# Kernel tuning notes

Hardware: AMD Instinct MI355X
Metric: run time of the kernel (lower is better)

## Reference

```python
import jax, jax.numpy as jnp
import numpy as np

B, T = 64, 1024
FRAME, ENC, HID = 512, 256, 512
LN_EPS = 1e-5


def setup_inputs() -> dict:
    key = jax.random.key(0)
    ks = jax.random.split(key, 16)
    s = 0.05
    return {
        "x": jax.random.normal(ks[0], (B, FRAME, T), jnp.float32),
        "states_hc": jax.random.normal(ks[1], (4, B, HID), jnp.float32) * s,
        "W_enc": jax.random.normal(ks[2], (ENC, FRAME), jnp.float32) * s,
        "ln_g": jnp.ones((ENC,), jnp.float32),
        "ln_b": jnp.zeros((ENC,), jnp.float32),
        "Wih1": jax.random.normal(ks[3], (4 * HID, ENC), jnp.float32) * s,
        "Whh1": jax.random.normal(ks[4], (4 * HID, HID), jnp.float32) * s,
        "bih1": jax.random.normal(ks[5], (4 * HID,), jnp.float32) * s,
        "bhh1": jax.random.normal(ks[6], (4 * HID,), jnp.float32) * s,
        "Wih2": jax.random.normal(ks[7], (4 * HID, HID), jnp.float32) * s,
        "Whh2": jax.random.normal(ks[8], (4 * HID, HID), jnp.float32) * s,
        "bih2": jax.random.normal(ks[9], (4 * HID,), jnp.float32) * s,
        "bhh2": jax.random.normal(ks[10], (4 * HID,), jnp.float32) * s,
        "Wlin": jax.random.normal(ks[11], (ENC, HID), jnp.float32) * s,
        "blin": jax.random.normal(ks[12], (ENC,), jnp.float32) * s,
        "W_dec": jax.random.normal(ks[13], (FRAME, ENC), jnp.float32) * s,
    }


def _lstm(x, h0, c0, Wih, Whh, bih, bhh):
    # x: [B,T,I]; PyTorch gate order i,f,g,o. Precompute input projections.
    pre = jnp.einsum("bti,gi->btg", x, Wih) + bih + bhh  # [B,T,4H]

    def step(carry, p):
        h, c = carry
        gates = p + h @ Whh.T
        i, f, g, o = jnp.split(gates, 4, axis=-1)
        c = jax.nn.sigmoid(f) * c + jax.nn.sigmoid(i) * jnp.tanh(g)
        h = jax.nn.sigmoid(o) * jnp.tanh(c)
        return (h, c), h

    (h, c), ys = jax.lax.scan(step, (h0, c0), pre.transpose(1, 0, 2))
    return ys.transpose(1, 0, 2), h, c  # [B,T,H]


def reference(x, states_hc, W_enc, ln_g, ln_b, Wih1, Whh1, bih1, bhh1,
              Wih2, Whh2, bih2, bhh2, Wlin, blin, W_dec):
    # encoder: conv1x1 over channels -> [B,ENC,T], then to [B,T,ENC]
    encoded = jnp.einsum("bct,oc->bto", x, W_enc)  # [B,T,ENC]
    mu = jnp.mean(encoded, axis=-1, keepdims=True)
    var = jnp.var(encoded, axis=-1, keepdims=True)
    enc_norm = (encoded - mu) / jnp.sqrt(var + LN_EPS) * ln_g + ln_b

    h1, c1 = states_hc[0], states_hc[1]
    h2, c2 = states_hc[2], states_hc[3]
    x1, h1, c1 = _lstm(enc_norm, h1, c1, Wih1, Whh1, bih1, bhh1)
    x2, h2, c2 = _lstm(x1, h2, c2, Wih2, Whh2, bih2, bhh2)
    # dropout is identity at inference
    mask = jax.nn.sigmoid(x2 @ Wlin.T + blin)  # [B,T,ENC]
    est = mask * encoded  # mask applied to un-normalized encoding
    decoded = jnp.einsum("bto,fo->bft", est, W_dec)  # [B,FRAME,T]
    states_out = jnp.stack([h1, c1, h2, c2], axis=0)  # [4,B,HID]
    return decoded, states_out
```

## Files before the change

kernel.cpp:

```cpp
#include <hip/hip_runtime.h>
#include <stdint.h>

#define B_ 64
#define T_ 1024
#define E_ 256
#define H_ 512
#define BH_ (B_*H_)
#define DEC_ELEMS ((size_t)B_*512*1024)

typedef __attribute__((ext_vector_type(8))) short bf16x8;
typedef __attribute__((ext_vector_type(4))) float f32x4;
typedef unsigned long long u64;

__device__ __forceinline__ unsigned short f2bf(float f) {
  union { float f; unsigned int u; } v; v.f = f;
  unsigned int r = (v.u + 0x7fffu + ((v.u >> 16) & 1u)) >> 16;
  return (unsigned short)r;
}
__device__ __forceinline__ float bf2f(unsigned short s) {
  union { float f; unsigned int u; } v; v.u = ((unsigned int)s) << 16;
  return v.f;
}
__device__ __forceinline__ float sigf(float x) { return 1.f/(1.f + __expf(-x)); }
__device__ __forceinline__ float tanhfast(float x) {
  float e = __expf(2.f*x);
  return 1.f - 2.f/(e + 1.f);
}
__device__ __forceinline__ void st4bf(unsigned short* p, float4 v) {
  ushort4 u; u.x=f2bf(v.x); u.y=f2bf(v.y); u.z=f2bf(v.z); u.w=f2bf(v.w);
  *(ushort4*)p = u;
}
__device__ __forceinline__ u64 ld_dc64(const unsigned short* p) {
  return __hip_atomic_load((const u64*)p, __ATOMIC_RELAXED, __HIP_MEMORY_SCOPE_AGENT);
}
__device__ __forceinline__ void st_dc64(unsigned short* p, u64 v) {
  __hip_atomic_store((u64*)p, v, __ATOMIC_RELAXED, __HIP_MEMORY_SCOPE_AGENT);
}

__device__ __forceinline__ void waitflags(const int* f, int target, int wv) {
  if ((threadIdx.x >> 6) == wv) {
    const int* p = f + (threadIdx.x & 63);
    for (;;) {
      int v = __hip_atomic_load(p, __ATOMIC_RELAXED, __HIP_MEMORY_SCOPE_AGENT);
      if (__all(v >= target)) break;
      __builtin_amdgcn_s_sleep(1);
    }
  }
  __syncthreads();
}

__global__ void k_prep(const float* __restrict__ Wenc, const float* __restrict__ Wlin,
                       const float* __restrict__ Wdec, const float* __restrict__ states,
                       unsigned short* __restrict__ wencb, unsigned short* __restrict__ wlinb,
                       unsigned short* __restrict__ wdecb,
                       unsigned short* h1bc, unsigned short* h2bc) {
  int i = blockIdx.x*256 + threadIdx.x;
  if (i < 131072) {
    wencb[i] = f2bf(Wenc[i]);
    wlinb[i] = f2bf(Wlin[i]);
    wdecb[i] = f2bf(Wdec[i]);
  }
  if (i < BH_/4) {
    float4 a  = *(const float4*)(states + (size_t)i*4);
    float4 b2 = *(const float4*)(states + (size_t)2*BH_ + (size_t)i*4);
    ushort4 ua; ua.x=f2bf(a.x);  ua.y=f2bf(a.y);  ua.z=f2bf(a.z);  ua.w=f2bf(a.w);
    ushort4 ub; ub.x=f2bf(b2.x); ub.y=f2bf(b2.y); ub.z=f2bf(b2.z); ub.w=f2bf(b2.w);
    st_dc64(&h1bc[BH_ + i*4], *(const u64*)&ua);
    st_dc64(&h2bc[BH_ + i*4], *(const u64*)&ub);
  }
}

__global__ __launch_bounds__(256) void k_enc(const float* __restrict__ x,
    const unsigned short* __restrict__ wencb, const float* __restrict__ lng,
    const float* __restrict__ lnb,
    unsigned short* __restrict__ enc_norm, unsigned short* __restrict__ encoded) {
  __shared__ __align__(16) unsigned short xs[16][520];
  __shared__ __align__(16) float es[16][265];
  const int bx = blockIdx.x;
  const int b = bx >> 6, tt = (bx & 63) << 4;
  const int tid = threadIdx.x;

  const float* xb = x + (size_t)b*512*1024 + tt;
  #pragma unroll
  for (int it = 0; it < 8; ++it) {
    int idx = tid + it*256;
    int c = idx >> 2, i4 = idx & 3;
    float4 v = *(const float4*)(xb + (size_t)c*1024 + i4*4);
    xs[i4*4+0][c]=f2bf(v.x); xs[i4*4+1][c]=f2bf(v.y);
    xs[i4*4+2][c]=f2bf(v.z); xs[i4*4+3][c]=f2bf(v.w);
  }
  __syncthreads();

  const int w = tid >> 6, lane = tid & 63;
  const int n16 = lane & 15, q = lane >> 4;
  f32x4 acc[4];
  #pragma unroll
  for (int i = 0; i < 4; ++i) acc[i] = (f32x4){0.f,0.f,0.f,0.f};
  for (int ks = 0; ks < 16; ++ks) {
    int k0 = ks*32 + q*8;
    bf16x8 af = *(const bf16x8*)&xs[n16][k0];
    #pragma unroll
    for (int i = 0; i < 4; ++i) {
      int o = (w*4+i)*16 + n16;
      bf16x8 bf = *(const bf16x8*)&wencb[(size_t)o*512 + k0];
      acc[i] = __builtin_amdgcn_mfma_f32_16x16x32_bf16(af, bf, acc[i], 0,0,0);
    }
  }
  #pragma unroll
  for (int i = 0; i < 4; ++i) {
    int o = (w*4+i)*16 + n16;
    #pragma unroll
    for (int r = 0; r < 4; ++r) es[q*4+r][o] = acc[i][r];
  }
  __syncthreads();

  const int tl = tid >> 4, l16 = tid & 15;
  float s = 0.f, ss = 0.f;
  #pragma unroll
  for (int k = 0; k < 16; ++k) { float v = es[tl][l16 + 16*k]; s += v; ss += v*v; }
  #pragma unroll
  for (int d = 1; d < 16; d <<= 1) { s += __shfl_xor(s, d, 64); ss += __shfl_xor(ss, d, 64); }
  float mu  = s  * (1.f/256.f);
  float var = ss * (1.f/256.f) - mu*mu;
  float rstd = rsqrtf(var + 1e-5f);
  #pragma unroll
  for (int k = 0; k < 16; ++k) {
    int o = l16 + 16*k;
    xs[tl][o] = f2bf((es[tl][o] - mu)*rstd*lng[o] + lnb[o]);
  }
  __syncthreads();
  #pragma unroll
  for (int it = 0; it < 2; ++it) {
    int idx = tid + it*256; int row = idx >> 5, ch = idx & 31;
    *(uint4*)&enc_norm[((size_t)(b*1024 + tt + row))*256 + ch*8] = *(const uint4*)&xs[row][ch*8];
  }
  __syncthreads();
  #pragma unroll
  for (int k = 0; k < 16; ++k) { int o = l16 + 16*k; xs[tl][o] = f2bf(es[tl][o]); }
  __syncthreads();
  #pragma unroll
  for (int it = 0; it < 2; ++it) {
    int idx = tid + it*256; int row = idx >> 5, ch = idx & 31;
    *(uint4*)&encoded[((size_t)(b*1024 + tt + row))*256 + ch*8] = *(const uint4*)&xs[row][ch*8];
  }
}

__global__ __launch_bounds__(256, 1) void k_recur(
    const float* __restrict__ states,
    const float* __restrict__ Wih1, const float* __restrict__ Whh1,
    const float* __restrict__ bih1, const float* __restrict__ bhh1,
    const float* __restrict__ Wih2, const float* __restrict__ Whh2,
    const float* __restrict__ bih2, const float* __restrict__ bhh2,
    const unsigned short* __restrict__ enc_norm,
    unsigned short* __restrict__ x2,
    unsigned short* h1bc, unsigned short* h2bc,
    int* flags1, int* flags2,
    float* __restrict__ out_states)
{
  __shared__ __align__(16) unsigned short wl1[32][776];
  __shared__ __align__(16) unsigned short wl2[32][1032];
  __shared__ __align__(16) unsigned short inA[16][1288];
  __shared__ float ps[2][32][17];
  __shared__ float cb[2][8][16];
  __shared__ float bias1[32], bias2[32];
  __shared__ __align__(8) unsigned short h1sh[16][8], h2sh[16][8];

  const int tid = threadIdx.x;
  const int g  = blockIdx.x & 3;
  const int j  = blockIdx.x >> 2;
  const int b0 = g*16;
  const int hc0 = j*8;
  int* f1 = flags1 + g*64;
  int* f2 = flags2 + g*64;

  for (int idx = tid; idx < 32*192; idx += 256) {
    int n = idx / 192, p = idx % 192;
    int R = (n>>3)*512 + hc0 + (n&7);
    if (p < 64) {
      st4bf(&wl1[n][p*4], *(const float4*)(Wih1 + (size_t)R*256 + p*4));
    } else {
      int p2 = p - 64;
      st4bf(&wl1[n][256 + p2*4], *(const float4*)(Whh1 + (size_t)R*512 + p2*4));
    }
  }
  for (int idx = tid; idx < 32*256; idx += 256) {
    int n = idx >> 8, p = idx & 255;
    int R = (n>>3)*512 + hc0 + (n&7);
    if (p < 128) {
      st4bf(&wl2[n][p*4], *(const float4*)(Wih2 + (size_t)R*512 + p*4));
    } else {
      int p2 = p - 128;
      st4bf(&wl2[n][512 + p2*4], *(const float4*)(Whh2 + (size_t)R*512 + p2*4));
    }
  }
  if (tid < 32) {
    int R = (tid>>3)*512 + hc0 + (tid&7);
    bias1[tid] = bih1[R] + bhh1[R];
    bias2[tid] = bih2[R] + bhh2[R];
  }
  if (tid < 128) {
    int b = tid & 15, hc = tid >> 4;
    cb[0][hc][b] = states[(size_t)1*BH_ + (b0+b)*H_ + hc0+hc];
    cb[1][hc][b] = states[(size_t)3*BH_ + (b0+b)*H_ + hc0+hc];
  }
  __syncthreads();

  const int w = tid >> 6, lane = tid & 63;
  const int n16 = lane & 15, q = lane >> 4;
  const int nt = w & 1, kh = w >> 1;

  for (int t = 0; t < T_; ++t) {
    const int pc = t & 1, pr = pc ^ 1;

    #pragma unroll
    for (int it = 0; it < 2; ++it) {
      int idx = tid + it*256;
      int b = idx >> 5, p = idx & 31;
      *(uint4*)&inA[b][p*8] = *(const uint4*)&enc_norm[((size_t)(b0+b)*T_ + t)*E_ + p*8];
    }
    if (t >= 1) waitflags(f1, t, 1);
    {
      u64 tmp[8];
      #pragma unroll
      for (int it = 0; it < 8; ++it) {
        int idx = tid + it*256; int b = idx >> 7, p = idx & 127;
        tmp[it] = ld_dc64(&h1bc[(size_t)pr*BH_ + (b0+b)*H_ + p*4]);
      }
      #pragma unroll
      for (int it = 0; it < 8; ++it) {
        int idx = tid + it*256; int b = idx >> 7, p = idx & 127;
        *(u64*)&inA[b][256 + p*4] = tmp[it];
      }
    }
    __syncthreads();

    {
      f32x4 acc = (f32x4){0.f,0.f,0.f,0.f};
      #pragma unroll
      for (int ks = 0; ks < 12; ++ks) {
        int k0 = kh*384 + ks*32 + q*8;
        bf16x8 af = *(const bf16x8*)&inA[n16][k0];
        bf16x8 bf = *(const bf16x8*)&wl1[nt*16 + n16][k0];
        acc = __builtin_amdgcn_mfma_f32_16x16x32_bf16(af, bf, acc, 0,0,0);
      }
      #pragma unroll
      for (int r = 0; r < 4; ++r) ps[kh][nt*16+n16][q*4+r] = acc[r];
    }
    __syncthreads();
    if (tid < 128) {
      int b = tid & 15, hc = tid >> 4;
      float ip = ps[0][hc][b]    + ps[1][hc][b]    + bias1[hc];
      float fp = ps[0][8+hc][b]  + ps[1][8+hc][b]  + bias1[8+hc];
      float gp = ps[0][16+hc][b] + ps[1][16+hc][b] + bias1[16+hc];
      float op = ps[0][24+hc][b] + ps[1][24+hc][b] + bias1[24+hc];
      float c = sigf(fp)*cb[0][hc][b] + sigf(ip)*tanhfast(gp);
      cb[0][hc][b] = c;
      float h = sigf(op)*tanhfast(c);
      h1sh[b][hc] = f2bf(h);
      if (t == T_-1) {
        out_states[(size_t)0*BH_ + (b0+b)*H_ + hc0+hc] = h;
        out_states[(size_t)1*BH_ + (b0+b)*H_ + hc0+hc] = c;
      }
    }
    __syncthreads();
    if (tid < 32) {
      int b = tid & 15, qq = tid >> 4;
      st_dc64(&h1bc[(size_t)pc*BH_ + (b0+b)*H_ + hc0 + qq*4], *(const u64*)&h1sh[b][qq*4]);
    }
    if (tid < 64) {
      asm volatile("s_waitcnt vmcnt(0)" ::: "memory");
      if (tid == 0)
        __hip_atomic_store(&f1[j], t+1, __ATOMIC_RELAXED, __HIP_MEMORY_SCOPE_AGENT);
    }

    if (t >= 2) waitflags(f2, t-1, 2);
    if (t >= 1) {
      u64 tmp[8];
      #pragma unroll
      for (int it = 0; it < 8; ++it) {
        int idx = tid + it*256; int b = idx >> 7, p = idx & 127;
        tmp[it] = ld_dc64(&h2bc[(size_t)pc*BH_ + (b0+b)*H_ + p*4]);
      }
      #pragma unroll
      for (int it = 0; it < 8; ++it) {
        int idx = tid + it*256; int b = idx >> 7, p = idx & 127;
        *(u64*)&inA[b][768 + p*4] = tmp[it];
      }
    }
    __syncthreads();

    if (t >= 1) {
      {
        f32x4 acc = (f32x4){0.f,0.f,0.f,0.f};
        #pragma unroll
        for (int ks = 0; ks < 16; ++ks) {
          int k0 = kh*512 + ks*32 + q*8;
          bf16x8 af = *(const bf16x8*)&inA[n16][256 + k0];
          bf16x8 bf = *(const bf16x8*)&wl2[nt*16 + n16][k0];
          acc = __builtin_amdgcn_mfma_f32_16x16x32_bf16(af, bf, acc, 0,0,0);
        }
        #pragma unroll
        for (int r = 0; r < 4; ++r) ps[kh][nt*16+n16][q*4+r] = acc[r];
      }
      __syncthreads();
      if (tid < 128) {
        int b = tid & 15, hc = tid >> 4;
        float ip = ps[0][hc][b]    + ps[1][hc][b]    + bias2[hc];
        float fp = ps[0][8+hc][b]  + ps[1][8+hc][b]  + bias2[8+hc];
        float gp = ps[0][16+hc][b] + ps[1][16+hc][b] + bias2[16+hc];
        float op = ps[0][24+hc][b] + ps[1][24+hc][b] + bias2[24+hc];
        float c = sigf(fp)*cb[1][hc][b] + sigf(ip)*tanhfast(gp);
        cb[1][hc][b] = c;
        float h = sigf(op)*tanhfast(c);
        h2sh[b][hc] = f2bf(h);
      }
      __syncthreads();
      if (tid < 32) {
        int b = tid & 15, qq = tid >> 4;
        u64 v = *(const u64*)&h2sh[b][qq*4];
        st_dc64(&h2bc[(size_t)pr*BH_ + (b0+b)*H_ + hc0 + qq*4], v);
        *(u64*)&x2[((size_t)(b0+b)*T_ + (t-1))*H_ + hc0 + qq*4] = v;
      }
      if (tid < 64) {
        asm volatile("s_waitcnt vmcnt(0)" ::: "memory");
        if (tid == 0)
          __hip_atomic_store(&f2[j], t, __ATOMIC_RELAXED, __HIP_MEMORY_SCOPE_AGENT);
      }
    }
  }

  {
    waitflags(f1, T_, 1);
    {
      u64 tmp[8];
      #pragma unroll
      for (int it = 0; it < 8; ++it) {
        int idx = tid + it*256; int b = idx >> 7, p = idx & 127;
        tmp[it] = ld_dc64(&h1bc[(size_t)1*BH_ + (b0+b)*H_ + p*4]);
      }
      #pragma unroll
      for (int it = 0; it < 8; ++it) {
        int idx = tid + it*256; int b = idx >> 7, p = idx & 127;
        *(u64*)&inA[b][256 + p*4] = tmp[it];
      }
    }
    waitflags(f2, T_-1, 2);
    {
      u64 tmp[8];
      #pragma unroll
      for (int it = 0; it < 8; ++it) {
        int idx = tid + it*256; int b = idx >> 7, p = idx & 127;
        tmp[it] = ld_dc64(&h2bc[(size_t)0*BH_ + (b0+b)*H_ + p*4]);
      }
      #pragma unroll
      for (int it = 0; it < 8; ++it) {
        int idx = tid + it*256; int b = idx >> 7, p = idx & 127;
        *(u64*)&inA[b][768 + p*4] = tmp[it];
      }
    }
    __syncthreads();
    {
      f32x4 acc = (f32x4){0.f,0.f,0.f,0.f};
      #pragma unroll
      for (int ks = 0; ks < 16; ++ks) {
        int k0 = kh*512 + ks*32 + q*8;
        bf16x8 af = *(const bf16x8*)&inA[n16][256 + k0];
        bf16x8 bf = *(const bf16x8*)&wl2[nt*16 + n16][k0];
        acc = __builtin_amdgcn_mfma_f32_16x16x32_bf16(af, bf, acc, 0,0,0);
      }
      #pragma unroll
      for (int r = 0; r < 4; ++r) ps[kh][nt*16+n16][q*4+r] = acc[r];
    }
    __syncthreads();
    if (tid < 128) {
      int b = tid & 15, hc = tid >> 4;
      float ip = ps[0][hc][b]    + ps[1][hc][b]    + bias2[hc];
      float fp = ps[0][8+hc][b]  + ps[1][8+hc][b]  + bias2[8+hc];
      float gp = ps[0][16+hc][b] + ps[1][16+hc][b] + bias2[16+hc];
      float op = ps[0][24+hc][b] + ps[1][24+hc][b] + bias2[24+hc];
      float c = sigf(fp)*cb[1][hc][b] + sigf(ip)*tanhfast(gp);
      float h = sigf(op)*tanhfast(c);
      h2sh[b][hc] = f2bf(h);
      out_states[(size_t)2*BH_ + (b0+b)*H_ + hc0+hc] = h;
      out_states[(size_t)3*BH_ + (b0+b)*H_ + hc0+hc] = c;
    }
    __syncthreads();
    if (tid < 32) {
      int b = tid & 15, qq = tid >> 4;
      *(u64*)&x2[((size_t)(b0+b)*T_ + (T_-1))*H_ + hc0 + qq*4] = *(const u64*)&h2sh[b][qq*4];
    }
  }
}

__global__ __launch_bounds__(256) void k_mask(const unsigned short* __restrict__ x2,
    const unsigned short* __restrict__ wlinb, const float* __restrict__ blin,
    unsigned short* __restrict__ est) {
  const int bx = blockIdx.x;
  const int b = bx >> 6, tt = (bx & 63) << 4;
  const int tid = threadIdx.x, w = tid >> 6, lane = tid & 63;
  const int n16 = lane & 15, q = lane >> 4;
  f32x4 acc[4];
  #pragma unroll
  for (int i = 0; i < 4; ++i) acc[i] = (f32x4){0.f,0.f,0.f,0.f};
  const unsigned short* arow = x2 + ((size_t)b*1024 + tt)*512;
  for (int ks = 0; ks < 16; ++ks) {
    int k0 = ks*32 + q*8;
    bf16x8 af = *(const bf16x8*)&arow[(size_t)n16*512 + k0];
    #pragma unroll
    for (int i = 0; i < 4; ++i) {
      int o = (w*4+i)*16 + n16;
      bf16x8 bf = *(const bf16x8*)&wlinb[(size_t)o*512 + k0];
      acc[i] = __builtin_amdgcn_mfma_f32_16x16x32_bf16(af, bf, acc[i], 0,0,0);
    }
  }
  #pragma unroll
  for (int i = 0; i < 4; ++i) {
    int o = (w*4+i)*16 + n16;
    float bl = blin[o];
    #pragma unroll
    for (int r = 0; r < 4; ++r) {
      size_t p = ((size_t)b*1024 + tt + q*4 + r)*256 + o;
      float m = sigf(acc[i][r] + bl);
      est[p] = f2bf(m * bf2f(est[p]));
    }
  }
}

__global__ __launch_bounds__(256) void k_dec(const unsigned short* __restrict__ est,
    const unsigned short* __restrict__ wdecb, float* __restrict__ dec) {
  const int bx = blockIdx.x;
  const int b = bx >> 7, rem = bx & 127, fy = rem >> 4, tx = rem & 15;
  const int f0 = fy*64, t0 = tx*64;
  const int tid = threadIdx.x, w = tid >> 6, lane = tid & 63;
  const int n16 = lane & 15, q = lane >> 4;
  f32x4 acc[4];
  #pragma unroll
  for (int i = 0; i < 4; ++i) acc[i] = (f32x4){0.f,0.f,0.f,0.f};
  const int fr = f0 + w*16 + n16;
  for (int ks = 0; ks < 8; ++ks) {
    int k0 = ks*32 + q*8;
    bf16x8 af = *(const bf16x8*)&wdecb[(size_t)fr*256 + k0];
    #pragma unroll
    for (int i = 0; i < 4; ++i) {
      int trow = t0 + i*16 + n16;
      bf16x8 bf = *(const bf16x8*)&est[((size_t)b*1024 + trow)*256 + k0];
      acc[i] = __builtin_amdgcn_mfma_f32_16x16x32_bf16(af, bf, acc[i], 0,0,0);
    }
  }
  #pragma unroll
  for (int i = 0; i < 4; ++i) {
    int tcol = t0 + i*16 + n16;
    #pragma unroll
    for (int r = 0; r < 4; ++r) {
      int f = f0 + w*16 + q*4 + r;
      dec[((size_t)b*512 + f)*1024 + tcol] = acc[i][r];
    }
  }
}

extern "C" void kernel_launch(void* const* d_in, const int* in_sizes, int n_in,
                              void* d_out, int out_size, void* d_ws, size_t ws_size,
                              hipStream_t stream) {
  (void)in_sizes; (void)n_in; (void)out_size; (void)ws_size;
  const float* x      = (const float*)d_in[0];
  const float* states = (const float*)d_in[1];
  const float* Wenc   = (const float*)d_in[2];
  const float* lng    = (const float*)d_in[3];
  const float* lnb    = (const float*)d_in[4];
  const float* Wih1   = (const float*)d_in[5];
  const float* Whh1   = (const float*)d_in[6];
  const float* bih1   = (const float*)d_in[7];
  const float* bhh1   = (const float*)d_in[8];
  const float* Wih2   = (const float*)d_in[9];
  const float* Whh2   = (const float*)d_in[10];
  const float* bih2   = (const float*)d_in[11];
  const float* bhh2   = (const float*)d_in[12];
  const float* Wlin   = (const float*)d_in[13];
  const float* blin   = (const float*)d_in[14];
  const float* Wdec   = (const float*)d_in[15];

  float* dec = (float*)d_out;
  float* out_states = dec + DEC_ELEMS;

  char* ws = (char*)d_ws;
  unsigned short* enc_norm = (unsigned short*)ws; ws += (size_t)B_*T_*E_*2;
  unsigned short* encoded  = (unsigned short*)ws; ws += (size_t)B_*T_*E_*2;
  unsigned short* x2buf    = (unsigned short*)ws; ws += (size_t)B_*T_*H_*2;
  unsigned short* wencb    = (unsigned short*)ws; ws += 131072*2;
  unsigned short* wlinb    = (unsigned short*)ws; ws += 131072*2;
  unsigned short* wdecb    = (unsigned short*)ws; ws += 131072*2;
  unsigned short* h1bc     = (unsigned short*)ws; ws += 2*BH_*2;
  unsigned short* h2bc     = (unsigned short*)ws; ws += 2*BH_*2;
  int* flags               = (int*)ws;            ws += 2*4*64*4;

  (void)hipMemsetAsync(flags, 0, 2*4*64*4, stream);
  k_prep<<<512, 256, 0, stream>>>(Wenc, Wlin, Wdec, states, wencb, wlinb, wdecb, h1bc, h2bc);
  k_enc<<<4096, 256, 0, stream>>>(x, wencb, lng, lnb, enc_norm, encoded);
  k_recur<<<256, 256, 0, stream>>>(states, Wih1, Whh1, bih1, bhh1,
                                   Wih2, Whh2, bih2, bhh2,
                                   enc_norm, x2buf, h1bc, h2bc,
                                   flags, flags + 4*64, out_states);
  k_mask<<<4096, 256, 0, stream>>>(x2buf, wlinb, blin, encoded);
  k_dec<<<8192, 256, 0, stream>>>(encoded, wdecb, dec);
}
```

Baseline: 4.772 ms.

## Restructure LSTM recurrence step into warp-specialized phases with fewer barriers

```diff
diff --git a/kernel.cpp b/kernel.cpp
--- a/kernel.cpp
+++ b/kernel.cpp
@@ -35,6 +35,9 @@
 }
 __device__ __forceinline__ void st_dc64(unsigned short* p, u64 v) {
   __hip_atomic_store((u64*)p, v, __ATOMIC_RELAXED, __HIP_MEMORY_SCOPE_AGENT);
+}
+__device__ __forceinline__ void st_dc32(unsigned short* p, unsigned int v) {
+  __hip_atomic_store((unsigned int*)p, v, __ATOMIC_RELAXED, __HIP_MEMORY_SCOPE_AGENT);
 }
 
 __device__ __forceinline__ void waitflags(const int* f, int target, int wv) {
@@ -160,10 +163,8 @@
   __shared__ __align__(16) unsigned short wl1[32][776];
   __shared__ __align__(16) unsigned short wl2[32][1032];
   __shared__ __align__(16) unsigned short inA[16][1288];
-  __shared__ float ps[2][32][17];
-  __shared__ float cb[2][8][16];
-  __shared__ float bias1[32], bias2[32];
-  __shared__ __align__(8) unsigned short h1sh[16][8], h2sh[16][8];
+  __shared__ float gbuf1[32][17];
+  __shared__ float gbuf2[32][17];
 
   const int tid = threadIdx.x;
   const int g  = blockIdx.x & 3;
@@ -193,31 +194,38 @@
       st4bf(&wl2[n][512 + p2*4], *(const float4*)(Whh2 + (size_t)R*512 + p2*4));
     }
   }
-  if (tid < 32) {
-    int R = (tid>>3)*512 + hc0 + (tid&7);
-    bias1[tid] = bih1[R] + bhh1[R];
-    bias2[tid] = bih2[R] + bhh2[R];
-  }
-  if (tid < 128) {
-    int b = tid & 15, hc = tid >> 4;
-    cb[0][hc][b] = states[(size_t)1*BH_ + (b0+b)*H_ + hc0+hc];
-    cb[1][hc][b] = states[(size_t)3*BH_ + (b0+b)*H_ + hc0+hc];
-  }
-  __syncthreads();
 
   const int w = tid >> 6, lane = tid & 63;
   const int n16 = lane & 15, q = lane >> 4;
-  const int nt = w & 1, kh = w >> 1;
+
+  const int bE = lane & 15;
+  const int hp = lane >> 4;
+  float cb1[2], cb2[2], b1r[4][2], b2r[4][2];
+  if (w == 0) {
+    #pragma unroll
+    for (int e = 0; e < 2; ++e) {
+      int col = hc0 + 2*hp + e;
+      cb1[e] = states[(size_t)1*BH_ + (b0+bE)*H_ + col];
+      cb2[e] = states[(size_t)3*BH_ + (b0+bE)*H_ + col];
+      #pragma unroll
+      for (int gi = 0; gi < 4; ++gi) {
+        int R = gi*512 + col;
+        b1r[gi][e] = bih1[R] + bhh1[R];
+        b2r[gi][e] = bih2[R] + bhh2[R];
+      }
+    }
+  }
+
+  #pragma unroll
+  for (int it = 0; it < 2; ++it) {
+    int idx = tid + it*256;
+    int b = idx >> 5, p = idx & 31;
+    *(uint4*)&inA[b][p*8] = *(const uint4*)&enc_norm[((size_t)(b0+b)*T_ + 0)*E_ + p*8];
+  }
 
   for (int t = 0; t < T_; ++t) {
     const int pc = t & 1, pr = pc ^ 1;
 
-    #pragma unroll
-    for (int it = 0; it < 2; ++it) {
-      int idx = tid + it*256;
-      int b = idx >> 5, p = idx & 31;
-      *(uint4*)&inA[b][p*8] = *(const uint4*)&enc_norm[((size_t)(b0+b)*T_ + t)*E_ + p*8];
-    }
     if (t >= 1) waitflags(f1, t, 1);
     {
       u64 tmp[8];
@@ -226,6 +234,14 @@
         int idx = tid + it*256; int b = idx >> 7, p = idx & 127;
         tmp[it] = ld_dc64(&h1bc[(size_t)pr*BH_ + (b0+b)*H_ + p*4]);
       }
+      if (w >= 2 && t >= 2) {
+        const int* p = f2 + lane;
+        for (;;) {
+          int v = __hip_atomic_load(p, __ATOMIC_RELAXED, __HIP_MEMORY_SCOPE_AGENT);
+          if (__all(v >= t-1)) break;
+          __builtin_amdgcn_s_sleep(1);
+        }
+      }
       #pragma unroll
       for (int it = 0; it < 8; ++it) {
         int idx = tid + it*256; int b = idx >> 7, p = idx & 127;
@@ -234,98 +250,110 @@
     }
     __syncthreads();
 
-    {
-      f32x4 acc = (f32x4){0.f,0.f,0.f,0.f};
+    if (w < 2) {
+      const int nt = w;
+      f32x4 a0 = (f32x4){0.f,0.f,0.f,0.f};
+      f32x4 a1 = (f32x4){0.f,0.f,0.f,0.f};
       #pragma unroll
       for (int ks = 0; ks < 12; ++ks) {
-        int k0 = kh*384 + ks*32 + q*8;
-        bf16x8 af = *(const bf16x8*)&inA[n16][k0];
-        bf16x8 bf = *(const bf16x8*)&wl1[nt*16 + n16][k0];
-        acc = __builtin_amdgcn_mfma_f32_16x16x32_bf16(af, bf, acc, 0,0,0);
-      }
-      #pragma unroll
-      for (int r = 0; r < 4; ++r) ps[kh][nt*16+n16][q*4+r] = acc[r];
+        int k0 = ks*32 + q*8;
+        a0 = __builtin_amdgcn_mfma_f32_16x16x32_bf16(
+               *(const bf16x8*)&inA[n16][k0],
+               *(const bf16x8*)&wl1[nt*16 + n16][k0], a0, 0,0,0);
+        a1 = __builtin_amdgcn_mfma_f32_16x16x32_bf16(
+               *(const bf16x8*)&inA[n16][384 + k0],
+               *(const bf16x8*)&wl1[nt*16 + n16][384 + k0], a1, 0,0,0);
+      }
+      #pragma unroll
+      for (int r = 0; r < 4; ++r) gbuf1[nt*16 + n16][q*4+r] = a0[r] + a1[r];
+    } else if (t >= 1) {
+      int tl = tid - 128;
+      u64 tmp[16];
+      #pragma unroll
+      for (int it = 0; it < 16; ++it) {
+        int idx = tl + it*128; int b = idx >> 7, p = idx & 127;
+        tmp[it] = ld_dc64(&h2bc[(size_t)pc*BH_ + (b0+b)*H_ + p*4]);
+      }
+      #pragma unroll
+      for (int it = 0; it < 16; ++it) {
+        int idx = tl + it*128; int b = idx >> 7, p = idx & 127;
+        *(u64*)&inA[b][768 + p*4] = tmp[it];
+      }
     }
     __syncthreads();
-    if (tid < 128) {
-      int b = tid & 15, hc = tid >> 4;
-      float ip = ps[0][hc][b]    + ps[1][hc][b]    + bias1[hc];
-      float fp = ps[0][8+hc][b]  + ps[1][8+hc][b]  + bias1[8+hc];
-      float gp = ps[0][16+hc][b] + ps[1][16+hc][b] + bias1[16+hc];
-      float op = ps[0][24+hc][b] + ps[1][24+hc][b] + bias1[24+hc];
-      float c = sigf(fp)*cb[0][hc][b] + sigf(ip)*tanhfast(gp);
-      cb[0][hc][b] = c;
-      float h = sigf(op)*tanhfast(c);
-      h1sh[b][hc] = f2bf(h);
+
+    if (w == 0) {
+      float hv[2];
+      #pragma unroll
+      for (int e = 0; e < 2; ++e) {
+        int hc = 2*hp + e;
+        float ip = gbuf1[hc][bE]      + b1r[0][e];
+        float fp = gbuf1[8+hc][bE]    + b1r[1][e];
+        float gp = gbuf1[16+hc][bE]   + b1r[2][e];
+        float op = gbuf1[24+hc][bE]   + b1r[3][e];
+        float c = sigf(fp)*cb1[e] + sigf(ip)*tanhfast(gp);
+        cb1[e] = c;
+        hv[e] = sigf(op)*tanhfast(c);
+      }
+      unsigned int pk = (unsigned int)f2bf(hv[0]) | ((unsigned int)f2bf(hv[1]) << 16);
+      st_dc32(&h1bc[(size_t)pc*BH_ + (b0+bE)*H_ + hc0 + 2*hp], pk);
       if (t == T_-1) {
-        out_states[(size_t)0*BH_ + (b0+b)*H_ + hc0+hc] = h;
-        out_states[(size_t)1*BH_ + (b0+b)*H_ + hc0+hc] = c;
-      }
-    }
-    __syncthreads();
-    if (tid < 32) {
-      int b = tid & 15, qq = tid >> 4;
-      st_dc64(&h1bc[(size_t)pc*BH_ + (b0+b)*H_ + hc0 + qq*4], *(const u64*)&h1sh[b][qq*4]);
-    }
-    if (tid < 64) {
+        *(float2*)&out_states[(size_t)0*BH_ + (b0+bE)*H_ + hc0 + 2*hp] = make_float2(hv[0], hv[1]);
+        *(float2*)&out_states[(size_t)1*BH_ + (b0+bE)*H_ + hc0 + 2*hp] = make_float2(cb1[0], cb1[1]);
+      }
       asm volatile("s_waitcnt vmcnt(0)" ::: "memory");
       if (tid == 0)
         __hip_atomic_store(&f1[j], t+1, __ATOMIC_RELAXED, __HIP_MEMORY_SCOPE_AGENT);
-    }
-
-    if (t >= 2) waitflags(f2, t-1, 2);
-    if (t >= 1) {
-      u64 tmp[8];
-      #pragma unroll
-      for (int it = 0; it < 8; ++it) {
-        int idx = tid + it*256; int b = idx >> 7, p = idx & 127;
-        tmp[it] = ld_dc64(&h2bc[(size_t)pc*BH_ + (b0+b)*H_ + p*4]);
-      }
-      #pragma unroll
-      for (int it = 0; it < 8; ++it) {
-        int idx = tid + it*256; int b = idx >> 7, p = idx & 127;
-        *(u64*)&inA[b][768 + p*4] = tmp[it];
-      }
-    }
-    __syncthreads();
-
-    if (t >= 1) {
-      {
-        f32x4 acc = (f32x4){0.f,0.f,0.f,0.f};
+    } else if (w <= 2) {
+      if (t >= 1) {
+        const int nt = w - 1;
+        f32x4 a0 = (f32x4){0.f,0.f,0.f,0.f};
+        f32x4 a1 = (f32x4){0.f,0.f,0.f,0.f};
         #pragma unroll
         for (int ks = 0; ks < 16; ++ks) {
-          int k0 = kh*512 + ks*32 + q*8;
-          bf16x8 af = *(const bf16x8*)&inA[n16][256 + k0];
-          bf16x8 bf = *(const bf16x8*)&wl2[nt*16 + n16][k0];
-          acc = __builtin_amdgcn_mfma_f32_16x16x32_bf16(af, bf, acc, 0,0,0);
+          int k0 = ks*32 + q*8;
+          a0 = __builtin_amdgcn_mfma_f32_16x16x32_bf16(
+                 *(const bf16x8*)&inA[n16][256 + k0],
+                 *(const bf16x8*)&wl2[nt*16 + n16][k0], a0, 0,0,0);
+          a1 = __builtin_amdgcn_mfma_f32_16x16x32_bf16(
+                 *(const bf16x8*)&inA[n16][768 + k0],
+                 *(const bf16x8*)&wl2[nt*16 + n16][512 + k0], a1, 0,0,0);
         }
         #pragma unroll
-        for (int r = 0; r < 4; ++r) ps[kh][nt*16+n16][q*4+r] = acc[r];
-      }
-      __syncthreads();
-      if (tid < 128) {
-        int b = tid & 15, hc = tid >> 4;
-        float ip = ps[0][hc][b]    + ps[1][hc][b]    + bias2[hc];
-        float fp = ps[0][8+hc][b]  + ps[1][8+hc][b]  + bias2[8+hc];
-        float gp = ps[0][16+hc][b] + ps[1][16+hc][b] + bias2[16+hc];
-        float op = ps[0][24+hc][b] + ps[1][24+hc][b] + bias2[24+hc];
-        float c = sigf(fp)*cb[1][hc][b] + sigf(ip)*tanhfast(gp);
-        cb[1][hc][b] = c;
-        float h = sigf(op)*tanhfast(c);
-        h2sh[b][hc] = f2bf(h);
-      }
-      __syncthreads();
-      if (tid < 32) {
-        int b = tid & 15, qq = tid >> 4;
-        u64 v = *(const u64*)&h2sh[b][qq*4];
-        st_dc64(&h2bc[(size_t)pr*BH_ + (b0+b)*H_ + hc0 + qq*4], v);
-        *(u64*)&x2[((size_t)(b0+b)*T_ + (t-1))*H_ + hc0 + qq*4] = v;
-      }
-      if (tid < 64) {
-        asm volatile("s_waitcnt vmcnt(0)" ::: "memory");
-        if (tid == 0)
-          __hip_atomic_store(&f2[j], t, __ATOMIC_RELAXED, __HIP_MEMORY_SCOPE_AGENT);
-      }
+        for (int r = 0; r < 4; ++r) gbuf2[nt*16 + n16][q*4+r] = a0[r] + a1[r];
+      }
+    } else {
+      if (t+1 < T_) {
+        #pragma unroll
+        for (int it = 0; it < 8; ++it) {
+          int idx = lane + it*64;
+          int b = idx >> 5, p = idx & 31;
+          *(uint4*)&inA[b][p*8] =
+            *(const uint4*)&enc_norm[((size_t)(b0+b)*T_ + (t+1))*E_ + p*8];
+        }
+      }
+    }
+    __syncthreads();
+
+    if (w == 0 && t >= 1) {
+      float hv[2];
+      #pragma unroll
+      for (int e = 0; e < 2; ++e) {
+        int hc = 2*hp + e;
+        float ip = gbuf2[hc][bE]      + b2r[0][e];
+        float fp = gbuf2[8+hc][bE]    + b2r[1][e];
+        float gp = gbuf2[16+hc][bE]   + b2r[2][e];
+        float op = gbuf2[24+hc][bE]   + b2r[3][e];
+        float c = sigf(fp)*cb2[e] + sigf(ip)*tanhfast(gp);
+        cb2[e] = c;
+        hv[e] = sigf(op)*tanhfast(c);
+      }
+      unsigned int pk = (unsigned int)f2bf(hv[0]) | ((unsigned int)f2bf(hv[1]) << 16);
+      st_dc32(&h2bc[(size_t)pr*BH_ + (b0+bE)*H_ + hc0 + 2*hp], pk);
+      *(unsigned int*)&x2[((size_t)(b0+bE)*T_ + (t-1))*H_ + hc0 + 2*hp] = pk;
+      asm volatile("s_waitcnt vmcnt(0)" ::: "memory");
+      if (tid == 0)
+        __hip_atomic_store(&f2[j], t, __ATOMIC_RELAXED, __HIP_MEMORY_SCOPE_AGENT);
     }
   }
 
@@ -359,35 +387,41 @@
       }
     }
     __syncthreads();
-    {
-      f32x4 acc = (f32x4){0.f,0.f,0.f,0.f};
+    if (w == 1 || w == 2) {
+      const int nt = w - 1;
+      f32x4 a0 = (f32x4){0.f,0.f,0.f,0.f};
+      f32x4 a1 = (f32x4){0.f,0.f,0.f,0.f};
       #pragma unroll
       for (int ks = 0; ks < 16; ++ks) {
-        int k0 = kh*512 + ks*32 + q*8;
-        bf16x8 af = *(const bf16x8*)&inA[n16][256 + k0];
-        bf16x8 bf = *(const bf16x8*)&wl2[nt*16 + n16][k0];
-        acc = __builtin_amdgcn_mfma_f32_16x16x32_bf16(af, bf, acc, 0,0,0);
-      }
-      #pragma unroll
-      for (int r = 0; r < 4; ++r) ps[kh][nt*16+n16][q*4+r] = acc[r];
+        int k0 = ks*32 + q*8;
+        a0 = __builtin_amdgcn_mfma_f32_16x16x32_bf16(
+               *(const bf16x8*)&inA[n16][256 + k0],
+               *(const bf16x8*)&wl2[nt*16 + n16][k0], a0, 0,0,0);
+        a1 = __builtin_amdgcn_mfma_f32_16x16x32_bf16(
+               *(const bf16x8*)&inA[n16][768 + k0],
+               *(const bf16x8*)&wl2[nt*16 + n16][512 + k0], a1, 0,0,0);
+      }
+      #pragma unroll
+      for (int r = 0; r < 4; ++r) gbuf2[nt*16 + n16][q*4+r] = a0[r] + a1[r];
     }
     __syncthreads();
-    if (tid < 128) {
-      int b = tid & 15, hc = tid >> 4;
-      float ip = ps[0][hc][b]    + ps[1][hc][b]    + bias2[hc];
-      float fp = ps[0][8+hc][b]  + ps[1][8+hc][b]  + bias2[8+hc];
-      float gp = ps[0][16+hc][b] + ps[1][16+hc][b] + bias2[16+hc];
-      float op = ps[0][24+hc][b] + ps[1][24+hc][b] + bias2[24+hc];
-      float c = sigf(fp)*cb[1][hc][b] + sigf(ip)*tanhfast(gp);
-      float h = sigf(op)*tanhfast(c);
-      h2sh[b][hc] = f2bf(h);
-      out_states[(size_t)2*BH_ + (b0+b)*H_ + hc0+hc] = h;
-      out_states[(size_t)3*BH_ + (b0+b)*H_ + hc0+hc] = c;
-    }
-    __syncthreads();
-    if (tid < 32) {
-      int b = tid & 15, qq = tid >> 4;
-      *(u64*)&x2[((size_t)(b0+b)*T_ + (T_-1))*H_ + hc0 + qq*4] = *(const u64*)&h2sh[b][qq*4];
+    if (w == 0) {
+      float hv[2];
+      #pragma unroll
+      for (int e = 0; e < 2; ++e) {
+        int hc = 2*hp + e;
+        float ip = gbuf2[hc][bE]      + b2r[0][e];
+        float fp = gbuf2[8+hc][bE]    + b2r[1][e];
+        float gp = gbuf2[16+hc][bE]   + b2r[2][e];
+        float op = gbuf2[24+hc][bE]   + b2r[3][e];
+        float c = sigf(fp)*cb2[e] + sigf(ip)*tanhfast(gp);
+        cb2[e] = c;
+        hv[e] = sigf(op)*tanhfast(c);
+      }
+      unsigned int pk = (unsigned int)f2bf(hv[0]) | ((unsigned int)f2bf(hv[1]) << 16);
+      *(unsigned int*)&x2[((size_t)(b0+bE)*T_ + (T_-1))*H_ + hc0 + 2*hp] = pk;
+      *(float2*)&out_states[(size_t)2*BH_ + (b0+bE)*H_ + hc0 + 2*hp] = make_float2(hv[0], hv[1]);
+      *(float2*)&out_states[(size_t)3*BH_ + (b0+bE)*H_ + hc0 + 2*hp] = make_float2(cb2[0], cb2[1]);
     }
   }
 }
```

Measured after the change: 5.054 ms. 1.06x slower.
